# Kernel optimization log

Hardware: AMD Instinct MI355X
Metric: run time of the kernel (lower is better)

The kernel has to match this reference:

```python
import jax, jax.numpy as jnp
import numpy as np

NUM_FRAMES = 300
HEAD_SIZE = 4
ATT_SIZE = 64
HIDDEN = 64


def setup_inputs() -> dict:
    key = jax.random.key(0)
    ks = jax.random.split(key, 7)
    B, S, H = 16, 7500, HIDDEN
    HD = HEAD_SIZE * ATT_SIZE  # 256
    # xavier_uniform bound for Linear(in=H, out=HD): sqrt(6/(H+HD))
    b_qkv = float(np.sqrt(6.0 / (H + HD)))
    b_o = float(np.sqrt(6.0 / (HD + H)))
    return {
        "q": jax.random.normal(ks[0], (B, S, H), dtype=jnp.float32),
        "k": jax.random.normal(ks[1], (B, S, H), dtype=jnp.float32),
        "v": jax.random.normal(ks[2], (B, S, H), dtype=jnp.float32),
        # stored as (in, out) so application is x @ W (== torch x @ weight.T)
        "Wq": jax.random.uniform(ks[3], (H, HD), jnp.float32, -b_qkv, b_qkv),
        "Wk": jax.random.uniform(ks[4], (H, HD), jnp.float32, -b_qkv, b_qkv),
        "Wv": jax.random.uniform(ks[5], (H, HD), jnp.float32, -b_qkv, b_qkv),
        "Wo": jax.random.uniform(ks[6], (HD, H), jnp.float32, -b_o, b_o),
    }


def reference(q, k, v, Wq, Wk, Wv, Wo):
    B, S, H = q.shape
    T, hs, dk = NUM_FRAMES, HEAD_SIZE, ATT_SIZE
    J = S // T  # joint groups
    scale = dk ** (-0.5)

    def proj(x, W):
        # (B,S,H) -> (B,J,hs,T,dk)
        y = (x @ W).reshape(B, J, T, hs, dk)
        return jnp.swapaxes(y, -2, -3)

    qh = proj(q, Wq) * scale
    kh = proj(k, Wk)
    vh = proj(v, Wv)
    # attention over the frame axis, per (batch, joint-group, head)
    scores = jnp.einsum('bjhtd,bjhsd->bjhts', qh, kh)  # (B,J,hs,T,T)
    p = jax.nn.softmax(scores, axis=-1)
    out = jnp.einsum('bjhts,bjhsd->bjhtd', p, vh)  # (B,J,hs,T,dk)
    out = jnp.swapaxes(out, -2, -3).reshape(B, S, hs * dk)
    return out @ Wo  # (B,S,H)
```

## Files before the change

kernel.cpp:

```cpp
#include <hip/hip_runtime.h>
#include <hip/hip_bf16.h>

#define NB 16
#define SS 7500
#define HH 64
#define TT 300
#define NHEAD 4
#define DKV 64
#define NJ 25
#define HDW 256
#define NQT 19
#define NST 10

typedef __attribute__((ext_vector_type(8))) short short8;
typedef __attribute__((ext_vector_type(4))) short s16x4;
typedef __attribute__((ext_vector_type(4))) float f32x4;

__device__ inline short f2bf(float f) {
    union { float f; unsigned u; } x; x.f = f;
    unsigned u = x.u + 0x7FFFu + ((x.u >> 16) & 1u);
    return (short)(u >> 16);
}
__device__ inline unsigned pk2(float a, float b) {
    __hip_bfloat162 h = __float22bfloat162_rn(make_float2(a, b));
    union { __hip_bfloat162 h; unsigned u; } c; c.h = h; return c.u;
}
#define MFMA32(a, b, c) __builtin_amdgcn_mfma_f32_16x16x32_bf16((a), (b), (c), 0, 0, 0)
#define LGKM_BAR() asm volatile("s_waitcnt lgkmcnt(0)" ::: "memory")

__device__ __forceinline__ short8 pks8(unsigned a, unsigned b, unsigned c2, unsigned d) {
    union { uint4 u; short8 s; } c; c.u.x = a; c.u.y = b; c.u.z = c2; c.u.w = d; return c.s;
}
__device__ __forceinline__ short8 cat8(s16x4 a, s16x4 b) {
    return __builtin_shufflevector(a, b, 0, 1, 2, 3, 4, 5, 6, 7);
}
__device__ __forceinline__ short8 packx(const float* px) {
    const float4 x0 = *(const float4*)px;
    const float4 x1 = *(const float4*)(px + 4);
    union { uint4 u; short8 s; } cv;
    cv.u.x = pk2(x0.x, x0.y); cv.u.y = pk2(x0.z, x0.w);
    cv.u.z = pk2(x1.x, x1.y); cv.u.w = pk2(x1.z, x1.w);
    return cv.s;
}

#define WS_BYTES ((size_t)65536 * 2)
#define WOBASE 16384

__global__ void wfrag_kernel(const float* __restrict__ Wq, const float* __restrict__ Wk,
                             const float* __restrict__ Wv, const float* __restrict__ Wo,
                             unsigned short* __restrict__ ws) {
    const int f = blockIdx.x;
    const int lane = threadIdx.x;
    const int L15 = lane & 15, quad = lane >> 4;
    if (f < 32) {
        const int h = f >> 3, ntl = (f >> 1) & 3, kt = f & 1;
        const int c = ntl * 16 + L15;
        const int j = (c & 32) | ((c & 12) << 1) | ((c & 16) >> 2) | (c & 3);
        const float* wkp = Wk + j * HDW + h * 64;
        float acc[8] = {0.f, 0.f, 0.f, 0.f, 0.f, 0.f, 0.f, 0.f};
        for (int dd = 0; dd < 64; ++dd) {
            const float kv = wkp[dd];
            #pragma unroll
            for (int i = 0; i < 8; ++i)
                acc[i] += Wq[(kt * 32 + quad * 8 + i) * HDW + h * 64 + dd] * kv;
        }
        unsigned short* dst = ws + f * 512 + lane * 8;
        #pragma unroll
        for (int i = 0; i < 8; ++i)
            dst[i] = (unsigned short)f2bf(acc[i] * 0.125f);
    } else {
        const int g = f - 32, h = g >> 4, kc = (g >> 2) & 3, nc = g & 3;
        const int n = nc * 16 + L15;
        float acc[4] = {0.f, 0.f, 0.f, 0.f};
        for (int dd = 0; dd < 64; ++dd) {
            const float wo = Wo[(h * 64 + dd) * HH + n];
            #pragma unroll
            for (int i = 0; i < 4; ++i)
                acc[i] += Wv[(kc * 16 + quad * 4 + i) * HDW + h * 64 + dd] * wo;
        }
        unsigned short* dst = ws + WOBASE + g * 256 + lane * 4;
        #pragma unroll
        for (int i = 0; i < 4; ++i)
            dst[i] = (unsigned short)f2bf(acc[i]);
    }
}


__device__ __forceinline__ void qproj_reg(const short8 qx[2],
                                          const unsigned short* __restrict__ wf,
                                          int h, short8* qa8, int lane) {
    #pragma unroll
    for (int p = 0; p < 2; ++p) {
        unsigned pkv[4];
        #pragma unroll
        for (int hf = 0; hf < 2; ++hf) {
            const int ntl = 2 * p + hf;
            const short8 b0 = *(const short8*)&wf[((h * 4 + ntl) * 2 + 0) * 512 + lane * 8];
            const short8 b1 = *(const short8*)&wf[((h * 4 + ntl) * 2 + 1) * 512 + lane * 8];
            f32x4 c = {0.f, 0.f, 0.f, 0.f};
            c = MFMA32(b0, qx[0], c);
            c = MFMA32(b1, qx[1], c);
            pkv[2 * hf + 0] = pk2(c[0], c[1]);
            pkv[2 * hf + 1] = pk2(c[2], c[3]);
        }
        qa8[p] = pks8(pkv[0], pkv[1], pkv[2], pkv[3]);
    }
}

__device__ __forceinline__ void attn_pass2(const unsigned short* __restrict__ sK,
                                           const unsigned short* __restrict__ sV,
                                           const short8 qa8[2][2], f32x4 oT[2][4],
                                           float* __restrict__ lsum,
                                           int L15, int quad) {
    #pragma unroll 2
    for (int st = 0; st < NST; ++st) {
        unsigned ptw[2][4];
        #pragma unroll
        for (int rh = 0; rh < 2; ++rh) {
            int row = st * 32 + rh * 16 + L15; if (row > TT - 1) row = TT - 1;
            const int r7 = row & 7;
            const short8 k0 = *(const short8*)&sK[row * 64 + ((quad ^ r7) << 3)];
            const short8 k1 = *(const short8*)&sK[row * 64 + (((4 + quad) ^ r7) << 3)];
            #pragma unroll
            for (int su = 0; su < 2; ++su) {
                f32x4 c = {0.f, 0.f, 0.f, 0.f};
                c = MFMA32(k0, qa8[su][0], c);
                c = MFMA32(k1, qa8[su][1], c);
                if (st == NST - 1) {
                    if (rh == 1 || quad == 3) {
                        c[0] = -1e38f; c[1] = -1e38f; c[2] = -1e38f; c[3] = -1e38f;
                    }
                }
                const float p0 = __expf(c[0] - 16.f);
                const float p1 = __expf(c[1] - 16.f);
                const float p2 = __expf(c[2] - 16.f);
                const float p3 = __expf(c[3] - 16.f);
                lsum[su] += (p0 + p1) + (p2 + p3);
                ptw[su][2 * rh + 0] = pk2(p0, p1);
                ptw[su][2 * rh + 1] = pk2(p2, p3);
            }
        }
        const short8 pa0 = pks8(ptw[0][0], ptw[0][1], ptw[0][2], ptw[0][3]);
        const short8 pa1 = pks8(ptw[1][0], ptw[1][1], ptw[1][2], ptw[1][3]);
        #pragma unroll
        for (int nt = 0; nt < 4; ++nt) {
            const int d = nt * 16 + L15;
            const short8 vp = *(const short8*)&sV[d * 328 + st * 32 + quad * 8];
            oT[0][nt] = MFMA32(vp, pa0, oT[0][nt]);
            oT[1][nt] = MFMA32(vp, pa1, oT[1][nt]);
        }
    }
}

__device__ __forceinline__ void epilogue(const unsigned short* __restrict__ wf, int h,
                                         float lsum, const f32x4* oT, f32x4* y, int lane) {
    lsum += __shfl_xor(lsum, 16);
    lsum += __shfl_xor(lsum, 32);
    const float linv = 1.f / lsum;
    short8 oa8[2];
    #pragma unroll
    for (int p = 0; p < 2; ++p)
        oa8[p] = pks8(pk2(oT[2 * p][0] * linv, oT[2 * p][1] * linv),
                      pk2(oT[2 * p][2] * linv, oT[2 * p][3] * linv),
                      pk2(oT[2 * p + 1][0] * linv, oT[2 * p + 1][1] * linv),
                      pk2(oT[2 * p + 1][2] * linv, oT[2 * p + 1][3] * linv));
    #pragma unroll
    for (int nc = 0; nc < 4; ++nc) {
        #pragma unroll
        for (int p = 0; p < 2; ++p) {
            const s16x4 w0 = *(const s16x4*)&wf[WOBASE + (((h * 4 + 2 * p + 0) * 4 + nc) << 8) + (lane << 2)];
            const s16x4 w1 = *(const s16x4*)&wf[WOBASE + (((h * 4 + 2 * p + 1) * 4 + nc) << 8) + (lane << 2)];
            y[nc] = MFMA32(oa8[p], cat8(w0, w1), y[nc]);
        }
    }
}

__device__ __forceinline__ void store_tile(float* __restrict__ out, long xbase, int tile,
                                           const f32x4* y, int L15, int quad) {
    #pragma unroll
    for (int nc = 0; nc < 4; ++nc)
        #pragma unroll
        for (int rr = 0; rr < 4; ++rr) {
            const int row = tile * 16 + quad * 4 + rr;
            if (row < TT)
                out[xbase + (long)row * HH + nc * 16 + L15] = y[nc][rr];
        }
}

__global__ __launch_bounds__(640, 2)
void attn11(const float* __restrict__ q, const float* __restrict__ k,
            const float* __restrict__ v, const unsigned short* __restrict__ wf,
            float* __restrict__ out)
{
    __shared__ __align__(16) unsigned short sK[19200];
    __shared__ __align__(16) unsigned short sV[64 * 328];

    const int tid = threadIdx.x;
    const int w = tid >> 6, lane = tid & 63;
    const int L15 = lane & 15, quad = lane >> 4;
    const int bj = blockIdx.x;
    const int b = bj / NJ, j = bj % NJ;
    const long xbase = ((long)b * SS + (long)j * TT) * HH;

    for (int i = tid; i < 2560; i += 640) {
        const int d = i / 40, p = 288 + (i % 40);
        sV[d * 328 + p] = 0;
    }

    short8 qx[2][2];
    #pragma unroll
    for (int t = 0; t < 2; ++t) {
        int r = (2 * w + t) * 16 + L15; if (r > TT - 1) r = TT - 1;
        const float* px = q + xbase + (long)r * HH + quad * 8;
        qx[t][0] = packx(px);
        qx[t][1] = packx(px + 32);
    }

    f32x4 y[2][4];
    #pragma unroll
    for (int sl = 0; sl < 2; ++sl)
        #pragma unroll
        for (int n = 0; n < 4; ++n) { y[sl][n][0]=0.f; y[sl][n][1]=0.f; y[sl][n][2]=0.f; y[sl][n][3]=0.f; }

    __syncthreads();

    for (int ji = 0; ji < 4; ++ji) {
        const int jb = w + 10 * ji;
        if (jb >= 38) break;
        const int isV = jb >= 19;
        const int t = isV ? jb - 19 : jb;
        const int s = t * 16 + L15;
        const int r = s > TT - 1 ? TT - 1 : s;
        const float* X = isV ? v : k;
        const float* px = X + xbase + (long)r * HH + quad * 8;
        const short8 xf0 = packx(px);
        const short8 xf1 = packx(px + 32);
        if (s < TT) {
            if (!isV) {
                const int p0 = (quad ^ (s & 7)) << 3;
                const int p1 = ((4 + quad) ^ (s & 7)) << 3;
                *(short8*)&sK[s * 64 + p0] = xf0;
                *(short8*)&sK[s * 64 + p1] = xf1;
            } else {
                const int pos = (s & ~31) + ((s >> 2) & 3) * 8 + ((s >> 4) & 1) * 4 + (s & 3);
                const unsigned short* a0 = (const unsigned short*)&xf0;
                const unsigned short* a1 = (const unsigned short*)&xf1;
                #pragma unroll
                for (int jj = 0; jj < 8; ++jj) {
                    sV[(quad * 8 + jj) * 328 + pos]        = a0[jj];
                    sV[(quad * 8 + jj + 32) * 328 + pos]   = a1[jj];
                }
            }
        }
    }
    __syncthreads();

    for (int h = 0; h < NHEAD; ++h) {
        short8 qa8[2][2];
        qproj_reg(qx[0], wf, h, qa8[0], lane);
        qproj_reg(qx[1], wf, h, qa8[1], lane);

        f32x4 oT[2][4]; float ls[2] = {0.f, 0.f};
        #pragma unroll
        for (int su = 0; su < 2; ++su)
            #pragma unroll
            for (int n = 0; n < 4; ++n) { oT[su][n][0]=0.f; oT[su][n][1]=0.f; oT[su][n][2]=0.f; oT[su][n][3]=0.f; }
        attn_pass2(sK, sV, qa8, oT, ls, L15, quad);
        epilogue(wf, h, ls[0], oT[0], y[0], lane);
        epilogue(wf, h, ls[1], oT[1], y[1], lane);
    }

    store_tile(out, xbase, 2 * w + 0, y[0], L15, quad);
    store_tile(out, xbase, 2 * w + 1, y[1], L15, quad);
}

#define TPAD 320
#define KSTR 72
#define VSTR 328
#define WSTR 72
#define NWAVE 8
#define MAXTILE 3

__global__ __launch_bounds__(512, 1)
void mha_mfma(const float* __restrict__ q, const float* __restrict__ k,
              const float* __restrict__ v,
              const float* __restrict__ Wq, const float* __restrict__ Wk,
              const float* __restrict__ Wv, const float* __restrict__ Wo,
              float* __restrict__ out)
{
    __shared__ short sK [TPAD * KSTR];
    __shared__ short sVT[DKV * VSTR];
    __shared__ short sWq[DKV * WSTR];
    __shared__ short sWk[DKV * WSTR];
    __shared__ short sWv[DKV * WSTR];
    __shared__ short sWo[DKV * WSTR];
    __shared__ short sScrF[NWAVE][16 * KSTR];

    const int tid  = threadIdx.x;
    const int w    = tid >> 6;
    const int lane = tid & 63;
    const int L15  = lane & 15;
    const int quad = lane >> 4;

    const int blk = blockIdx.x;
    const int j = blk % NJ;
    const int b = blk / NJ;
    const long xbase = ((long)b * SS + (long)j * TT) * HH;

    for (int idx = tid; idx < 20 * KSTR; idx += 512) sK[300 * KSTR + idx] = 0;
    for (int idx = tid; idx < DKV * 32; idx += 512) {
        const int d = idx >> 5, c = 300 + (idx & 31);
        if (c < VSTR) sVT[d * VSTR + c] = 0;
    }

    int myT[MAXTILE]; int nMy = 0;
    for (int t = w; t < NQT; t += NWAVE) myT[nMy++] = t;

    f32x4 y[MAXTILE][4];
    #pragma unroll
    for (int a = 0; a < MAXTILE; ++a)
        #pragma unroll
        for (int n = 0; n < 4; ++n) { y[a][n][0]=0.f; y[a][n][1]=0.f; y[a][n][2]=0.f; y[a][n][3]=0.f; }

    for (int h = 0; h < NHEAD; ++h) {
        __syncthreads();
        for (int idx = tid; idx < 4096; idx += 512) {
            const int d = idx & 63;
            const int i = idx >> 6;
            sWq[d * WSTR + i] = f2bf(Wq[i * HDW + h * DKV + d]);
            sWk[d * WSTR + i] = f2bf(Wk[i * HDW + h * DKV + d]);
            sWv[d * WSTR + i] = f2bf(Wv[i * HDW + h * DKV + d]);
            sWo[d * WSTR + i] = f2bf(Wo[(h * DKV + i) * HH + d]);
        }
        __syncthreads();

        for (int jb = w; jb < 2 * NQT; jb += NWAVE) {
            const int   isV  = jb >= NQT;
            const int   tile = isV ? jb - NQT : jb;
            const float* X   = isV ? v : k;
            const short* sW  = isV ? sWv : sWk;
            int r = tile * 16 + L15; if (r > TT - 1) r = TT - 1;
            short8 afr[2];
            #pragma unroll
            for (int kt = 0; kt < 2; ++kt) {
                const float* px = X + xbase + (long)r * HH + kt * 32 + quad * 8;
                const float4 x0 = *(const float4*)px;
                const float4 x1 = *(const float4*)(px + 4);
                short8 a;
                a[0]=f2bf(x0.x); a[1]=f2bf(x0.y); a[2]=f2bf(x0.z); a[3]=f2bf(x0.w);
                a[4]=f2bf(x1.x); a[5]=f2bf(x1.y); a[6]=f2bf(x1.z); a[7]=f2bf(x1.w);
                afr[kt] = a;
            }
            #pragma unroll
            for (int nt = 0; nt < 4; ++nt) {
                f32x4 c; c[0]=0.f; c[1]=0.f; c[2]=0.f; c[3]=0.f;
                #pragma unroll
                for (int kt = 0; kt < 2; ++kt) {
                    const short8 bfr = *(const short8*)&sW[(nt*16 + L15) * WSTR + kt*32 + quad*8];
                    c = MFMA32(afr[kt], bfr, c);
                }
                #pragma unroll
                for (int rr = 0; rr < 4; ++rr) {
                    const int s = tile*16 + quad*4 + rr;
                    if (s < TT) {
                        const short bv = f2bf(c[rr]);
                        const int d = nt*16 + L15;
                        if (isV) sVT[d * VSTR + s] = bv;
                        else     sK [s * KSTR + d] = bv;
                    }
                }
            }
        }
        __syncthreads();

        for (int ti = 0; ti < nMy; ++ti) {
            const int tile = myT[ti];
            short8 qa[2];
            {
                int r = tile * 16 + L15; if (r > TT - 1) r = TT - 1;
                short8 afr[2];
                #pragma unroll
                for (int kt = 0; kt < 2; ++kt) {
                    const float* px = q + xbase + (long)r * HH + kt * 32 + quad * 8;
                    const float4 x0 = *(const float4*)px;
                    const float4 x1 = *(const float4*)(px + 4);
                    short8 a;
                    a[0]=f2bf(x0.x); a[1]=f2bf(x0.y); a[2]=f2bf(x0.z); a[3]=f2bf(x0.w);
                    a[4]=f2bf(x1.x); a[5]=f2bf(x1.y); a[6]=f2bf(x1.z); a[7]=f2bf(x1.w);
                    afr[kt] = a;
                }
                #pragma unroll
                for (int nt = 0; nt < 4; ++nt) {
                    f32x4 c; c[0]=0.f; c[1]=0.f; c[2]=0.f; c[3]=0.f;
                    #pragma unroll
                    for (int kt = 0; kt < 2; ++kt) {
                        const short8 bfr = *(const short8*)&sWq[(nt*16 + L15) * WSTR + kt*32 + quad*8];
                        c = MFMA32(afr[kt], bfr, c);
                    }
                    #pragma unroll
                    for (int rr = 0; rr < 4; ++rr)
                        sScrF[w][(quad*4+rr)*KSTR + nt*16 + L15] = f2bf(c[rr] * 0.125f);
                }
                LGKM_BAR();
                qa[0] = *(const short8*)&sScrF[w][L15*KSTR + quad*8];
                qa[1] = *(const short8*)&sScrF[w][L15*KSTR + 32 + quad*8];
            }

            float m[4] = {-3e38f, -3e38f, -3e38f, -3e38f};
            float l[4] = {0.f, 0.f, 0.f, 0.f};
            f32x4 o[4];
            #pragma unroll
            for (int nt = 0; nt < 4; ++nt) { o[nt][0]=0.f; o[nt][1]=0.f; o[nt][2]=0.f; o[nt][3]=0.f; }

            for (int st = 0; st < NST; ++st) {
                f32x4 s0, s1;
                s0[0]=0.f;s0[1]=0.f;s0[2]=0.f;s0[3]=0.f;
                s1[0]=0.f;s1[1]=0.f;s1[2]=0.f;s1[3]=0.f;
                #pragma unroll
                for (int kt = 0; kt < 2; ++kt) {
                    const short8 b0 = *(const short8*)&sK[(st*32      + L15) * KSTR + kt*32 + quad*8];
                    const short8 b1 = *(const short8*)&sK[(st*32 + 16 + L15) * KSTR + kt*32 + quad*8];
                    s0 = MFMA32(qa[kt], b0, s0);
                    s1 = MFMA32(qa[kt], b1, s1);
                }
                if (st == NST - 1) {
                    if (L15 >= 12) { s0[0]=-1e38f; s0[1]=-1e38f; s0[2]=-1e38f; s0[3]=-1e38f; }
                    s1[0]=-1e38f; s1[1]=-1e38f; s1[2]=-1e38f; s1[3]=-1e38f;
                }
                float corr[4];
                #pragma unroll
                for (int rr = 0; rr < 4; ++rr) {
                    float t = fmaxf(s0[rr], s1[rr]);
                    t = fmaxf(t, __shfl_xor(t, 1));
                    t = fmaxf(t, __shfl_xor(t, 2));
                    t = fmaxf(t, __shfl_xor(t, 4));
                    t = fmaxf(t, __shfl_xor(t, 8));
                    const float mn = fmaxf(m[rr], t);
                    corr[rr] = __expf(m[rr] - mn);
                    m[rr] = mn;
                    const float p0 = __expf(s0[rr] - mn);
                    const float p1 = __expf(s1[rr] - mn);
                    float rs = p0 + p1;
                    rs += __shfl_xor(rs, 1);
                    rs += __shfl_xor(rs, 2);
                    rs += __shfl_xor(rs, 4);
                    rs += __shfl_xor(rs, 8);
                    l[rr] = l[rr] * corr[rr] + rs;
                    sScrF[w][(quad*4+rr)*KSTR + L15]      = f2bf(p0);
                    sScrF[w][(quad*4+rr)*KSTR + 16 + L15] = f2bf(p1);
                }
                #pragma unroll
                for (int nt = 0; nt < 4; ++nt) {
                    o[nt][0] *= corr[0]; o[nt][1] *= corr[1];
                    o[nt][2] *= corr[2]; o[nt][3] *= corr[3];
                }
                LGKM_BAR();
                const short8 pa = *(const short8*)&sScrF[w][L15*KSTR + quad*8];
                #pragma unroll
                for (int nt = 0; nt < 4; ++nt) {
                    const short8 vb = *(const short8*)&sVT[(nt*16 + L15) * VSTR + st*32 + quad*8];
                    o[nt] = MFMA32(pa, vb, o[nt]);
                }
            }

            float linv[4];
            #pragma unroll
            for (int rr = 0; rr < 4; ++rr) linv[rr] = 1.f / l[rr];
            #pragma unroll
            for (int nt = 0; nt < 4; ++nt)
                #pragma unroll
                for (int rr = 0; rr < 4; ++rr)
                    sScrF[w][(quad*4+rr)*KSTR + nt*16 + L15] = f2bf(o[nt][rr] * linv[rr]);
            LGKM_BAR();
            const short8 oa0 = *(const short8*)&sScrF[w][L15*KSTR + quad*8];
            const short8 oa1 = *(const short8*)&sScrF[w][L15*KSTR + 32 + quad*8];
            #pragma unroll
            for (int nt = 0; nt < 4; ++nt) {
                const short8 w0 = *(const short8*)&sWo[(nt*16 + L15) * WSTR + quad*8];
                const short8 w1 = *(const short8*)&sWo[(nt*16 + L15) * WSTR + 32 + quad*8];
                y[ti][nt] = MFMA32(oa0, w0, y[ti][nt]);
                y[ti][nt] = MFMA32(oa1, w1, y[ti][nt]);
            }
        }
    }

    for (int ti = 0; ti < nMy; ++ti) {
        const int tile = myT[ti];
        #pragma unroll
        for (int nt = 0; nt < 4; ++nt)
            #pragma unroll
            for (int rr = 0; rr < 4; ++rr) {
                const int row = tile*16 + quad*4 + rr;
                if (row < TT)
                    out[xbase + (long)row * HH + nt*16 + L15] = y[ti][nt][rr];
            }
    }
}

extern "C" void kernel_launch(void* const* d_in, const int* in_sizes, int n_in,
                              void* d_out, int out_size, void* d_ws, size_t ws_size,
                              hipStream_t stream) {
    const float* q  = (const float*)d_in[0];
    const float* k  = (const float*)d_in[1];
    const float* v  = (const float*)d_in[2];
    const float* Wq = (const float*)d_in[3];
    const float* Wk = (const float*)d_in[4];
    const float* Wv = (const float*)d_in[5];
    const float* Wo = (const float*)d_in[6];
    float* out = (float*)d_out;

    if (ws_size >= WS_BYTES) {
        unsigned short* ws = (unsigned short*)d_ws;
        wfrag_kernel<<<96, 64, 0, stream>>>(Wq, Wk, Wv, Wo, ws);
        attn11<<<NB * NJ, 640, 0, stream>>>(q, k, v, ws, out);
    } else {
        mha_mfma<<<NB * NJ, 512, 0, stream>>>(q, k, v, Wq, Wk, Wv, Wo, out);
    }
}
```

Measured before the change: 225.9 us.

## Use 8 waves per block with tail tiles and fold log2e into exp2 softmax

The attention kernel drops from 10 to 8 waves per block. Each wave still processes two 16-row query tiles, and the first three waves then handle the remaining three tiles in a single-tile pass. The softmax scale now includes log2(e), so the kernel calls the hardware exp2 directly instead of __expf, and the fixed shift is rescaled to match. The aim is lower per-block thread overhead and cheaper exponentials, at the cost of load imbalance in the tail pass.

```diff
diff --git a/kernel.cpp b/kernel.cpp
--- a/kernel.cpp
+++ b/kernel.cpp
@@ -27,6 +27,7 @@
 }
 #define MFMA32(a, b, c) __builtin_amdgcn_mfma_f32_16x16x32_bf16((a), (b), (c), 0, 0, 0)
 #define LGKM_BAR() asm volatile("s_waitcnt lgkmcnt(0)" ::: "memory")
+#define EXP2(x) __builtin_amdgcn_exp2f(x)
 
 __device__ __forceinline__ short8 pks8(unsigned a, unsigned b, unsigned c2, unsigned d) {
     union { uint4 u; short8 s; } c; c.u.x = a; c.u.y = b; c.u.z = c2; c.u.w = d; return c.s;
@@ -45,6 +46,7 @@
 
 #define WS_BYTES ((size_t)65536 * 2)
 #define WOBASE 16384
+#define EXP2_SHIFT 23.083121f
 
 __global__ void wfrag_kernel(const float* __restrict__ Wq, const float* __restrict__ Wk,
                              const float* __restrict__ Wv, const float* __restrict__ Wo,
@@ -67,7 +69,7 @@
         unsigned short* dst = ws + f * 512 + lane * 8;
         #pragma unroll
         for (int i = 0; i < 8; ++i)
-            dst[i] = (unsigned short)f2bf(acc[i] * 0.125f);
+            dst[i] = (unsigned short)f2bf(acc[i] * 0.18033688f);
     } else {
         const int g = f - 32, h = g >> 4, kc = (g >> 2) & 3, nc = g & 3;
         const int n = nc * 16 + L15;
@@ -107,14 +109,15 @@
     }
 }
 
-__device__ __forceinline__ void attn_pass2(const unsigned short* __restrict__ sK,
-                                           const unsigned short* __restrict__ sV,
-                                           const short8 qa8[2][2], f32x4 oT[2][4],
-                                           float* __restrict__ lsum,
-                                           int L15, int quad) {
+template <int NSUB>
+__device__ __forceinline__ void attn_pass(const unsigned short* __restrict__ sK,
+                                          const unsigned short* __restrict__ sV,
+                                          const short8 qa8[][2], f32x4 oT[][4],
+                                          float* __restrict__ lsum,
+                                          int L15, int quad) {
     #pragma unroll 2
     for (int st = 0; st < NST; ++st) {
-        unsigned ptw[2][4];
+        unsigned ptw[NSUB][4];
         #pragma unroll
         for (int rh = 0; rh < 2; ++rh) {
             int row = st * 32 + rh * 16 + L15; if (row > TT - 1) row = TT - 1;
@@ -122,7 +125,7 @@
             const short8 k0 = *(const short8*)&sK[row * 64 + ((quad ^ r7) << 3)];
             const short8 k1 = *(const short8*)&sK[row * 64 + (((4 + quad) ^ r7) << 3)];
             #pragma unroll
-            for (int su = 0; su < 2; ++su) {
+            for (int su = 0; su < NSUB; ++su) {
                 f32x4 c = {0.f, 0.f, 0.f, 0.f};
                 c = MFMA32(k0, qa8[su][0], c);
                 c = MFMA32(k1, qa8[su][1], c);
@@ -131,23 +134,26 @@
                         c[0] = -1e38f; c[1] = -1e38f; c[2] = -1e38f; c[3] = -1e38f;
                     }
                 }
-                const float p0 = __expf(c[0] - 16.f);
-                const float p1 = __expf(c[1] - 16.f);
-                const float p2 = __expf(c[2] - 16.f);
-                const float p3 = __expf(c[3] - 16.f);
+                const float p0 = EXP2(c[0] - EXP2_SHIFT);
+                const float p1 = EXP2(c[1] - EXP2_SHIFT);
+                const float p2 = EXP2(c[2] - EXP2_SHIFT);
+                const float p3 = EXP2(c[3] - EXP2_SHIFT);
                 lsum[su] += (p0 + p1) + (p2 + p3);
                 ptw[su][2 * rh + 0] = pk2(p0, p1);
                 ptw[su][2 * rh + 1] = pk2(p2, p3);
             }
         }
-        const short8 pa0 = pks8(ptw[0][0], ptw[0][1], ptw[0][2], ptw[0][3]);
-        const short8 pa1 = pks8(ptw[1][0], ptw[1][1], ptw[1][2], ptw[1][3]);
+        short8 pa[NSUB];
+        #pragma unroll
+        for (int su = 0; su < NSUB; ++su)
+            pa[su] = pks8(ptw[su][0], ptw[su][1], ptw[su][2], ptw[su][3]);
         #pragma unroll
         for (int nt = 0; nt < 4; ++nt) {
             const int d = nt * 16 + L15;
             const short8 vp = *(const short8*)&sV[d * 328 + st * 32 + quad * 8];
-            oT[0][nt] = MFMA32(vp, pa0, oT[0][nt]);
-            oT[1][nt] = MFMA32(vp, pa1, oT[1][nt]);
+            #pragma unroll
+            for (int su = 0; su < NSUB; ++su)
+                oT[su][nt] = MFMA32(vp, pa[su], oT[su][nt]);
         }
     }
 }
@@ -187,8 +193,8 @@
         }
 }
 
-__global__ __launch_bounds__(640, 2)
-void attn11(const float* __restrict__ q, const float* __restrict__ k,
+__global__ __launch_bounds__(512, 2)
+void attn13(const float* __restrict__ q, const float* __restrict__ k,
             const float* __restrict__ v, const unsigned short* __restrict__ wf,
             float* __restrict__ out)
 {
@@ -202,7 +208,7 @@
     const int b = bj / NJ, j = bj % NJ;
     const long xbase = ((long)b * SS + (long)j * TT) * HH;
 
-    for (int i = tid; i < 2560; i += 640) {
+    for (int i = tid; i < 2560; i += 512) {
         const int d = i / 40, p = 288 + (i % 40);
         sV[d * 328 + p] = 0;
     }
@@ -210,7 +216,7 @@
     short8 qx[2][2];
     #pragma unroll
     for (int t = 0; t < 2; ++t) {
-        int r = (2 * w + t) * 16 + L15; if (r > TT - 1) r = TT - 1;
+        const int r = (2 * w + t) * 16 + L15;
         const float* px = q + xbase + (long)r * HH + quad * 8;
         qx[t][0] = packx(px);
         qx[t][1] = packx(px + 32);
@@ -224,8 +230,8 @@
 
     __syncthreads();
 
-    for (int ji = 0; ji < 4; ++ji) {
-        const int jb = w + 10 * ji;
+    for (int ji = 0; ji < 5; ++ji) {
+        const int jb = w + 8 * ji;
         if (jb >= 38) break;
         const int isV = jb >= 19;
         const int t = isV ? jb - 19 : jb;
@@ -265,13 +271,36 @@
         for (int su = 0; su < 2; ++su)
             #pragma unroll
             for (int n = 0; n < 4; ++n) { oT[su][n][0]=0.f; oT[su][n][1]=0.f; oT[su][n][2]=0.f; oT[su][n][3]=0.f; }
-        attn_pass2(sK, sV, qa8, oT, ls, L15, quad);
+        attn_pass<2>(sK, sV, qa8, oT, ls, L15, quad);
         epilogue(wf, h, ls[0], oT[0], y[0], lane);
         epilogue(wf, h, ls[1], oT[1], y[1], lane);
     }
-
     store_tile(out, xbase, 2 * w + 0, y[0], L15, quad);
     store_tile(out, xbase, 2 * w + 1, y[1], L15, quad);
+
+    if (w < 3) {
+        const int t3 = 16 + w;
+        short8 qx3[2];
+        {
+            int r = t3 * 16 + L15; if (r > TT - 1) r = TT - 1;
+            const float* px = q + xbase + (long)r * HH + quad * 8;
+            qx3[0] = packx(px);
+            qx3[1] = packx(px + 32);
+        }
+        f32x4 y3[4];
+        #pragma unroll
+        for (int n = 0; n < 4; ++n) { y3[n][0]=0.f; y3[n][1]=0.f; y3[n][2]=0.f; y3[n][3]=0.f; }
+        for (int h = 0; h < NHEAD; ++h) {
+            short8 qa3[1][2];
+            qproj_reg(qx3, wf, h, qa3[0], lane);
+            f32x4 o3[1][4]; float ls3[1] = {0.f};
+            #pragma unroll
+            for (int n = 0; n < 4; ++n) { o3[0][n][0]=0.f; o3[0][n][1]=0.f; o3[0][n][2]=0.f; o3[0][n][3]=0.f; }
+            attn_pass<1>(sK, sV, qa3, o3, ls3, L15, quad);
+            epilogue(wf, h, ls3[0], o3[0], y3, lane);
+        }
+        store_tile(out, xbase, t3, y3, L15, quad);
+    }
 }
 
 #define TPAD 320
@@ -512,7 +541,7 @@
     if (ws_size >= WS_BYTES) {
         unsigned short* ws = (unsigned short*)d_ws;
         wfrag_kernel<<<96, 64, 0, stream>>>(Wq, Wk, Wv, Wo, ws);
-        attn11<<<NB * NJ, 640, 0, stream>>>(q, k, v, ws, out);
+        attn13<<<NB * NJ, 512, 0, stream>>>(q, k, v, ws, out);
     } else {
         mha_mfma<<<NB * NJ, 512, 0, stream>>>(q, k, v, Wq, Wk, Wv, Wo, out);
     }
```

Result: faster. 205.5 us (-9.0%).
